# Optimization experiments

Hardware: AMD Instinct MI355X
Metric: run time of the kernel (lower is better)

Reference implementation:

```python
import jax, jax.numpy as jnp
import numpy as np

H = 8
D = 64
SCALER = 1.0 / np.sqrt(D).astype(np.float32)


def setup_inputs() -> dict:
    key = jax.random.key(0)
    k1, k2 = jax.random.split(key)
    B, N, C = 2, 256, 512
    x = jax.random.normal(k1, (B, N, C), dtype=jnp.float32)
    # Linear(C, 5C, bias=False): weight shape [5C, C], torch convention y = x @ W.T
    w = jax.random.normal(k2, (5 * C, C), dtype=jnp.float32) * 0.02
    return {"x": x, "w": w}


def reference(x, w):
    B, N, C = x.shape
    # projections: a, b, c, vj, vk each [B, H, N, D]
    wx = (x @ w.T).reshape(B, N, 5, H, D).transpose(2, 0, 3, 1, 4)
    a, b, c, vj, vk = wx[0], wx[1], wx[2], wx[3], wx[4]

    # three pairwise score matrices, each [B, H, N, N]
    X = jnp.einsum('bhjd,bhkd->bhjk', b, c) * SCALER
    Y = jnp.einsum('bhkd,bhid->bhki', c, a) * SCALER
    Z = jnp.einsum('bhid,bhjd->bhij', a, b) * SCALER

    # custom 3-way softmax stabilization: X uses global max over (j,k),
    # Y uses max over k (axis -2), Z uses max over j (axis -1)
    X = jnp.exp(X - jnp.max(X, axis=(-2, -1), keepdims=True))
    Y = jnp.exp(Y - jnp.max(Y, axis=-2, keepdims=True))
    Z = jnp.exp(Z - jnp.max(Z, axis=-1, keepdims=True))

    # Num_{bhid} = sum_{j,k} Z_ij * X_jk * vj_jd * Y_ki * vk_kd
    # (same math as the original 5D 'bhjkd'/'bhikd' chain, fused via einsum path)
    Num = jnp.einsum('bhij,bhjk,bhjd,bhki,bhkd->bhid', Z, X, vj, Y, vk)
    # Den_{bhi} = sum_{j,k} Z_ij * Y_ki * X_jk
    Den = jnp.einsum('bhij,bhki,bhjk->bhi', Z, Y, X) + 1e-9

    att = Num / Den[..., None]                     # [B, H, N, D]
    att = att.transpose(0, 2, 1, 3).reshape(B, N, C)
    return att
```

## Files before the change

kernel.cpp:

```cpp
#include <hip/hip_runtime.h>
#include <math.h>

#define Bn 2
#define Hn 8
#define Nn 256
#define Dn 64
#define BH 16
#define SCALER 0.125f

typedef _Float16 half8 __attribute__((ext_vector_type(8)));
typedef _Float16 half4 __attribute__((ext_vector_type(4)));
typedef float floatx4 __attribute__((ext_vector_type(4)));

__device__ __forceinline__ void split_f32(float v, _Float16& h, _Float16& l) {
    h = (_Float16)v;
    l = (_Float16)(v - (float)h);
}

__device__ __forceinline__ void split8(const float4& v0, const float4& v1,
                                       half8& h, half8& l) {
    const float vv[8] = {v0.x, v0.y, v0.z, v0.w, v1.x, v1.y, v1.z, v1.w};
    #pragma unroll
    for (int e = 0; e < 8; ++e) {
        _Float16 hh, ll;
        split_f32(vv[e], hh, ll);
        h[e] = hh; l[e] = ll;
    }
}

__device__ __forceinline__ void gload_lds16(const float* g, void* lds_base) {
    __builtin_amdgcn_global_load_lds(
        (const __attribute__((address_space(1))) unsigned int*)g,
        (__attribute__((address_space(3))) unsigned int*)lds_base, 16, 0, 0);
}

__global__ __launch_bounds__(256) void split2_kernel(
    const float* __restrict__ x, const float* __restrict__ w,
    _Float16* __restrict__ xh, _Float16* __restrict__ xl,
    _Float16* __restrict__ wh, _Float16* __restrict__ wl) {
    const int b = blockIdx.x;
    const float* src;
    _Float16 *hp, *lp;
    int idx;
    if (b < 256) {
        idx = (b * 256 + threadIdx.x) * 4;
        src = x; hp = xh; lp = xl;
    } else {
        idx = ((b - 256) * 256 + threadIdx.x) * 4;
        src = w; hp = wh; lp = wl;
    }
    const float4 v = *(const float4*)(src + idx);
    half4 hh, ll;
    _Float16 a2, b2;
    split_f32(v.x, a2, b2); hh[0] = a2; ll[0] = b2;
    split_f32(v.y, a2, b2); hh[1] = a2; ll[1] = b2;
    split_f32(v.z, a2, b2); hh[2] = a2; ll[2] = b2;
    split_f32(v.w, a2, b2); hh[3] = a2; ll[3] = b2;
    *(half4*)(hp + idx) = hh;
    *(half4*)(lp + idx) = ll;
}

__global__ __launch_bounds__(256) void proj_mfma(
    const _Float16* __restrict__ xh, const _Float16* __restrict__ xl,
    const _Float16* __restrict__ wh, const _Float16* __restrict__ wl,
    float* __restrict__ P32) {
    const int m0 = blockIdx.x * 64;
    const int r0 = blockIdx.y * 64;
    const int t = threadIdx.x;
    const int w = t >> 6, l = t & 63;
    const int lr = l & 15, kk8 = (l >> 4) * 8;

    floatx4 acc[4];
    #pragma unroll
    for (int ni = 0; ni < 4; ++ni) acc[ni] = (floatx4){0.f, 0.f, 0.f, 0.f};

    const int arow = m0 + w * 16 + lr;
    for (int kt = 0; kt < 16; ++kt) {
        const int k0 = kt * 32 + kk8;
        const half8 ah = *(const half8*)(xh + arow * 512 + k0);
        const half8 al = *(const half8*)(xl + arow * 512 + k0);
        half8 bhv[4], blv[4];
        #pragma unroll
        for (int ni = 0; ni < 4; ++ni) {
            const int wr = r0 + ni * 16 + lr;
            bhv[ni] = *(const half8*)(wh + wr * 512 + k0);
            blv[ni] = *(const half8*)(wl + wr * 512 + k0);
        }
        #pragma unroll
        for (int ni = 0; ni < 4; ++ni)
            acc[ni] = __builtin_amdgcn_mfma_f32_16x16x32_f16(ah, bhv[ni], acc[ni], 0, 0, 0);
        #pragma unroll
        for (int ni = 0; ni < 4; ++ni)
            acc[ni] = __builtin_amdgcn_mfma_f32_16x16x32_f16(ah, blv[ni], acc[ni], 0, 0, 0);
        #pragma unroll
        for (int ni = 0; ni < 4; ++ni)
            acc[ni] = __builtin_amdgcn_mfma_f32_16x16x32_f16(al, bhv[ni], acc[ni], 0, 0, 0);
    }
    const int rbase = (l >> 4) * 4;
    #pragma unroll
    for (int ni = 0; ni < 4; ++ni) {
        const int rcol = r0 + ni * 16 + lr;
        const int s = rcol >> 9, h = (rcol >> 6) & 7, d = rcol & 63;
        #pragma unroll
        for (int r = 0; r < 4; ++r) {
            const int m = m0 + w * 16 + rbase + r;
            const int b = m >> 8, n = m & 255;
            P32[(((s * 2 + b) * 8 + h) * 256 + n) * 64 + d] = acc[ni][r];
        }
    }
}

__global__ __launch_bounds__(256) void score_vkt(
    const float* __restrict__ P32,
    _Float16* __restrict__ Xsh, _Float16* __restrict__ Xsl,
    float* __restrict__ Yt, float* __restrict__ Z, float* __restrict__ vkT) {
    const int bh = blockIdx.x, mat = blockIdx.y;
    const int t = threadIdx.x;
    if (mat == 3) {
        const int idx0 = blockIdx.z * 2048 + t * 8;
        const int d = idx0 >> 8, k0 = idx0 & 255;
        const float* src = P32 + (4 * 16 + bh) * 16384;
        float4 o0, o1;
        o0.x = src[(k0 + 0) * 64 + d]; o0.y = src[(k0 + 1) * 64 + d];
        o0.z = src[(k0 + 2) * 64 + d]; o0.w = src[(k0 + 3) * 64 + d];
        o1.x = src[(k0 + 4) * 64 + d]; o1.y = src[(k0 + 5) * 64 + d];
        o1.z = src[(k0 + 6) * 64 + d]; o1.w = src[(k0 + 7) * 64 + d];
        *(float4*)(vkT + (bh * 64 + d) * 256 + k0) = o0;
        *(float4*)(vkT + (bh * 64 + d) * 256 + k0 + 4) = o1;
        return;
    }
    const int i0 = (blockIdx.z >> 2) * 128;
    const int j0 = (blockIdx.z & 3) * 64;
    const int w = t >> 6, l = t & 63;
    const int lr = l & 15, kk8 = (l >> 4) * 8;
    const float* A;
    const float* Bm;
    if (mat == 0)      { A = P32 + (1 * 16 + bh) * 16384; Bm = P32 + (2 * 16 + bh) * 16384; }
    else if (mat == 1) { A = P32 + (0 * 16 + bh) * 16384; Bm = P32 + (2 * 16 + bh) * 16384; }
    else               { A = P32 + (0 * 16 + bh) * 16384; Bm = P32 + (1 * 16 + bh) * 16384; }

    floatx4 acc[2][4];
    #pragma unroll
    for (int mi = 0; mi < 2; ++mi)
        #pragma unroll
        for (int ni = 0; ni < 4; ++ni) acc[mi][ni] = (floatx4){0.f, 0.f, 0.f, 0.f};

    for (int kt = 0; kt < 2; ++kt) {
        const int k0 = kt * 32 + kk8;
        half8 ah[2], al[2], bh8[4], bl8[4];
        #pragma unroll
        for (int mi = 0; mi < 2; ++mi) {
            const int row = i0 + w * 32 + mi * 16 + lr;
            const float4 v0 = *(const float4*)(A + row * 64 + k0);
            const float4 v1 = *(const float4*)(A + row * 64 + k0 + 4);
            split8(v0, v1, ah[mi], al[mi]);
        }
        #pragma unroll
        for (int ni = 0; ni < 4; ++ni) {
            const int row = j0 + ni * 16 + lr;
            const float4 v0 = *(const float4*)(Bm + row * 64 + k0);
            const float4 v1 = *(const float4*)(Bm + row * 64 + k0 + 4);
            split8(v0, v1, bh8[ni], bl8[ni]);
        }
        #pragma unroll
        for (int mi = 0; mi < 2; ++mi)
            #pragma unroll
            for (int ni = 0; ni < 4; ++ni)
                acc[mi][ni] = __builtin_amdgcn_mfma_f32_16x16x32_f16(ah[mi], bh8[ni], acc[mi][ni], 0, 0, 0);
        #pragma unroll
        for (int mi = 0; mi < 2; ++mi)
            #pragma unroll
            for (int ni = 0; ni < 4; ++ni)
                acc[mi][ni] = __builtin_amdgcn_mfma_f32_16x16x32_f16(ah[mi], bl8[ni], acc[mi][ni], 0, 0, 0);
        #pragma unroll
        for (int mi = 0; mi < 2; ++mi)
            #pragma unroll
            for (int ni = 0; ni < 4; ++ni)
                acc[mi][ni] = __builtin_amdgcn_mfma_f32_16x16x32_f16(al[mi], bh8[ni], acc[mi][ni], 0, 0, 0);
    }
    const int rbase = (l >> 4) * 4;
    #pragma unroll
    for (int mi = 0; mi < 2; ++mi)
        #pragma unroll
        for (int ni = 0; ni < 4; ++ni)
            #pragma unroll
            for (int r = 0; r < 4; ++r) {
                const int row = i0 + w * 32 + mi * 16 + rbase + r;
                const int col = j0 + ni * 16 + lr;
                const float e = expf(acc[mi][ni][r] * SCALER);
                if (mat == 0) {
                    const int idx = (bh * 256 + row) * 256 + col;
                    _Float16 hh, ll; split_f32(e, hh, ll);
                    Xsh[idx] = hh; Xsl[idx] = ll;
                } else if (mat == 1) {
                    Yt[bh * 65536 + row * 256 + col] = e;
                } else {
                    Z[bh * 65536 + row * 256 + col] = e;
                }
            }
}

__global__ __launch_bounds__(256) void den_mfma(
    const float* __restrict__ Yt, const _Float16* __restrict__ Xh,
    const _Float16* __restrict__ Xl, const float* __restrict__ Z,
    float* __restrict__ Den) {
    const int bh = blockIdx.x;
    const int ibase = blockIdx.y * 16;
    const int t = threadIdx.x;
    const int w = t >> 6, l = t & 63;
    const int lr = l & 15, ks = l >> 4, kk8 = ks * 8;
    const float* Ytp = Yt + bh * 65536;
    const _Float16* Xhp = Xh + bh * 65536;
    const _Float16* Xlp = Xl + bh * 65536;

    floatx4 acc[4];
    #pragma unroll
    for (int q = 0; q < 4; ++q) acc[q] = (floatx4){0.f, 0.f, 0.f, 0.f};

    for (int kt = 0; kt < 8; ++kt) {
        const int k0 = kt * 32 + kk8;
        half8 ah, al;
        {
            const float4 v0 = *(const float4*)(Ytp + (ibase + lr) * 256 + k0);
            const float4 v1 = *(const float4*)(Ytp + (ibase + lr) * 256 + k0 + 4);
            split8(v0, v1, ah, al);
        }
        half8 bh8[4], bl8[4];
        #pragma unroll
        for (int q = 0; q < 4; ++q) {
            const int jt = w * 4 + q;
            bh8[q] = *(const half8*)(Xhp + (jt * 16 + lr) * 256 + k0);
            bl8[q] = *(const half8*)(Xlp + (jt * 16 + lr) * 256 + k0);
        }
        #pragma unroll
        for (int q = 0; q < 4; ++q)
            acc[q] = __builtin_amdgcn_mfma_f32_16x16x32_f16(ah, bh8[q], acc[q], 0, 0, 0);
        #pragma unroll
        for (int q = 0; q < 4; ++q)
            acc[q] = __builtin_amdgcn_mfma_f32_16x16x32_f16(ah, bl8[q], acc[q], 0, 0, 0);
        #pragma unroll
        for (int q = 0; q < 4; ++q)
            acc[q] = __builtin_amdgcn_mfma_f32_16x16x32_f16(al, bh8[q], acc[q], 0, 0, 0);
    }
    __shared__ float redS[4][16];
    float dp[4] = {0.f, 0.f, 0.f, 0.f};
    const float* Zp = Z + (bh * 256 + ibase) * 256;
    #pragma unroll
    for (int q = 0; q < 4; ++q) {
        const int jt = w * 4 + q;
        #pragma unroll
        for (int r = 0; r < 4; ++r)
            dp[r] += acc[q][r] * Zp[(ks * 4 + r) * 256 + jt * 16 + lr];
    }
    #pragma unroll
    for (int r = 0; r < 4; ++r) {
        float s = dp[r];
        s += __shfl_xor(s, 1); s += __shfl_xor(s, 2);
        s += __shfl_xor(s, 4); s += __shfl_xor(s, 8);
        if (lr == 0) redS[w][ks * 4 + r] = s;
    }
    __syncthreads();
    if (t < 16)
        Den[bh * 256 + ibase + t] =
            redS[0][t] + redS[1][t] + redS[2][t] + redS[3][t] + 1e-9f;
}

__global__ __launch_bounds__(256, 2) void attn_mfma(
    const _Float16* __restrict__ Xh, const _Float16* __restrict__ Xl,
    const float* __restrict__ Yt, const float* __restrict__ Z,
    const float* __restrict__ vkT, const float* __restrict__ P32,
    const float* __restrict__ Den, float* __restrict__ out) {
    const int id = (blockIdx.x & 7) * 256 + (blockIdx.x >> 3);
    const int bh = id >> 7;
    const int i0 = (id & 127) * 2;
    const int t = threadIdx.x;
    const int w = t >> 6, l = t & 63;
    const int lr = l & 15, ks = l >> 4, kk8 = ks * 8;

    __shared__ float yiS[2][256], ziS[2][256];
    __shared__ float RAW[2][2048];
    __shared__ _Float16 BhS[2][2][2048], BlS[2][2][2048];
    float (*redN)[2][64] = reinterpret_cast<float (*)[2][64]>(&yiS[0][0]);

    yiS[0][t] = Yt[(bh * 256 + i0) * 256 + t];
    yiS[1][t] = Yt[(bh * 256 + i0 + 1) * 256 + t];
    ziS[0][t] = Z[(bh * 256 + i0) * 256 + t];
    ziS[1][t] = Z[(bh * 256 + i0 + 1) * 256 + t];

    const _Float16* Xhp = Xh + bh * 65536;
    const _Float16* Xlp = Xl + bh * 65536;
    const float* vkp = vkT + bh * 16384;
    const float* vj = P32 + (3 * 16 + bh) * 16384;

    floatx4 acc[4][8];
    #pragma unroll
    for (int mi = 0; mi < 4; ++mi)
        #pragma unroll
        for (int ct = 0; ct < 8; ++ct) acc[mi][ct] = (floatx4){0.f, 0.f, 0.f, 0.f};

    const int bi = t >> 7;
    const int bd = (t >> 1) & 63;
    const int hf = t & 1;
    const int bs2 = hf * 2;

    auto STAGE = [&](int kt) {
        const int k0 = (kt & 7) * 32;
        const int buf = kt & 1;
        #pragma unroll
        for (int q = 0; q < 2; ++q) {
            const int u = q * 256 + t;
            const int g = u >> 7, ubd = (u & 127) >> 1, uhf = u & 1;
            const float* gp = vkp + ubd * 256 + k0 + uhf * 16 + g * 4;
            void* lp = (char*)&RAW[buf][0] + q * 4096 + w * 1024;
            gload_lds16(gp, lp);
        }
    };
    auto BSTORE = [&](int kt) {
        const int buf = kt & 1;
        const float* yrow = &yiS[bi][(kt & 7) * 32 + bs2 * 8];
        float4 V[4];
        #pragma unroll
        for (int g = 0; g < 4; ++g)
            V[g] = *(float4*)&RAW[buf][g * 512 + bd * 8 + hf * 4];
        #pragma unroll
        for (int g = 0; g < 2; ++g) {
            const float4 y0 = *(const float4*)(yrow + g * 8);
            const float4 y1 = *(const float4*)(yrow + g * 8 + 4);
            const float4 v0 = V[g * 2], v1 = V[g * 2 + 1];
            const float pv[8] = {v0.x * y0.x, v0.y * y0.y, v0.z * y0.z, v0.w * y0.w,
                                 v1.x * y1.x, v1.y * y1.y, v1.z * y1.z, v1.w * y1.w};
            half8 hv, lv;
            #pragma unroll
            for (int e = 0; e < 8; ++e) {
                _Float16 hh, ll;
                split_f32(pv[e], hh, ll);
                hv[e] = hh; lv[e] = ll;
            }
            const int off = ((bd * 4 + bs2 + g) ^ ((bd >> 1) & 7)) * 8;
            *(half8*)&BhS[buf][bi][off] = hv;
            *(half8*)&BlS[buf][bi][off] = lv;
        }
    };
    auto LOADA = [&](half8* AH, half8* AL, int kt) {
        const int k0 = (kt & 7) * 32 + kk8;
        #pragma unroll
        for (int mi = 0; mi < 4; ++mi) {
            const int row = w * 64 + mi * 16 + lr;
            AH[mi] = *(const half8*)(Xhp + row * 256 + k0);
            AL[mi] = *(const half8*)(Xlp + row * 256 + k0);
        }
    };
    auto MFMA_STEP = [&](half8* AH, half8* AL, int buf) {
        __builtin_amdgcn_s_setprio(1);
        #pragma unroll
        for (int ct = 0; ct < 8; ++ct) {
            const int ii = ct >> 2;
            const int dd = (ct & 3) * 16 + lr;
            const int off = ((dd * 4 + ks) ^ ((dd >> 1) & 7)) * 8;
            const half8 bhf = *(const half8*)&BhS[buf][ii][off];
            const half8 blf = *(const half8*)&BlS[buf][ii][off];
            #pragma unroll
            for (int mi = 0; mi < 4; ++mi)
                acc[mi][ct] = __builtin_amdgcn_mfma_f32_16x16x32_f16(AH[mi], bhf, acc[mi][ct], 0, 0, 0);
            #pragma unroll
            for (int mi = 0; mi < 4; ++mi)
                acc[mi][ct] = __builtin_amdgcn_mfma_f32_16x16x32_f16(AH[mi], blf, acc[mi][ct], 0, 0, 0);
            #pragma unroll
            for (int mi = 0; mi < 4; ++mi)
                acc[mi][ct] = __builtin_amdgcn_mfma_f32_16x16x32_f16(AL[mi], bhf, acc[mi][ct], 0, 0, 0);
        }
        __builtin_amdgcn_s_setprio(0);
    };

    half8 A0h[4], A0l[4], A1h[4], A1l[4];

    STAGE(0);
    STAGE(1);
    LOADA(A0h, A0l, 0);
    asm volatile("s_waitcnt vmcnt(10)" ::: "memory");
    __builtin_amdgcn_sched_barrier(0);
    asm volatile("s_waitcnt lgkmcnt(0)" ::: "memory");
    __builtin_amdgcn_s_barrier();
    BSTORE(0);
    asm volatile("s_waitcnt lgkmcnt(0)" ::: "memory");
    __builtin_amdgcn_s_barrier();

    #pragma unroll 1
    for (int kq = 0; kq < 4; ++kq) {
        const int kt = kq * 2;
        STAGE(kt + 2);
        LOADA(A1h, A1l, kt + 1);
        MFMA_STEP(A0h, A0l, 0);
        asm volatile("s_waitcnt vmcnt(18)" ::: "memory");
        __builtin_amdgcn_sched_barrier(0);
        BSTORE(kt + 1);
        asm volatile("s_waitcnt lgkmcnt(0)" ::: "memory");
        __builtin_amdgcn_s_barrier();
        STAGE(kt + 3);
        LOADA(A0h, A0l, kt + 2);
        MFMA_STEP(A1h, A1l, 1);
        if (kq < 3) {
            asm volatile("s_waitcnt vmcnt(18)" ::: "memory");
            __builtin_amdgcn_sched_barrier(0);
            BSTORE(kt + 2);
            asm volatile("s_waitcnt lgkmcnt(0)" ::: "memory");
            __builtin_amdgcn_s_barrier();
        }
    }

    float z0[16], z1[16];
    #pragma unroll
    for (int mi = 0; mi < 4; ++mi)
        #pragma unroll
        for (int r = 0; r < 4; ++r) {
            const int j = w * 64 + mi * 16 + ks * 4 + r;
            z0[mi * 4 + r] = ziS[0][j];
            z1[mi * 4 + r] = ziS[1][j];
        }
    #pragma unroll
    for (int dt = 0; dt < 4; ++dt) {
        float n0 = 0.f, n1 = 0.f;
        #pragma unroll
        for (int mi = 0; mi < 4; ++mi)
            #pragma unroll
            for (int r = 0; r < 4; ++r) {
                const int j = w * 64 + mi * 16 + ks * 4 + r;
                const float v = vj[j * 64 + dt * 16 + lr];
                n0 += acc[mi][dt][r] * z0[mi * 4 + r] * v;
                n1 += acc[mi][dt + 4][r] * z1[mi * 4 + r] * v;
            }
        n0 += __shfl_xor(n0, 16); n0 += __shfl_xor(n0, 32);
        n1 += __shfl_xor(n1, 16); n1 += __shfl_xor(n1, 32);
        if (l < 16) {
            redN[w][0][dt * 16 + l] = n0;
            redN[w][1][dt * 16 + l] = n1;
        }
    }
    __syncthreads();
    if (t < 128) {
        const int ih = t >> 6, d = t & 63;
        const float num = redN[0][ih][d] + redN[1][ih][d] +
                          redN[2][ih][d] + redN[3][ih][d];
        const int i = i0 + ih;
        const float den = Den[bh * 256 + i];
        out[((bh >> 3) * 256 + i) * 512 + (bh & 7) * 64 + d] = num / den;
    }
}

extern "C" void kernel_launch(void* const* d_in, const int* in_sizes, int n_in,
                              void* d_out, int out_size, void* d_ws, size_t ws_size,
                              hipStream_t stream) {
    const float* x = (const float*)d_in[0];
    const float* w = (const float*)d_in[1];
    float* out = (float*)d_out;

    float* ws = (float*)d_ws;
    float* P32 = ws;
    float* U = ws + 1310720;
    _Float16* xh = (_Float16*)U;
    _Float16* xl = xh + 262144;
    _Float16* wh = xl + 262144;
    _Float16* wl = wh + 1310720;
    _Float16* Xsh = (_Float16*)U;
    _Float16* Xsl = Xsh + 1048576;
    float* Yt = U + 1048576;
    float* Z = Yt + 1048576;
    float* vkT = Z + 1048576;
    float* Den = vkT + 262144;

    split2_kernel<<<1536, 256, 0, stream>>>(x, w, xh, xl, wh, wl);
    proj_mfma<<<dim3(8, 40), 256, 0, stream>>>(xh, xl, wh, wl, P32);
    score_vkt<<<dim3(16, 4, 8), 256, 0, stream>>>(P32, Xsh, Xsl, Yt, Z, vkT);
    den_mfma<<<dim3(16, 16), 256, 0, stream>>>(Yt, Xsh, Xsl, Z, Den);
    attn_mfma<<<2048, 256, 0, stream>>>(Xsh, Xsl, Yt, Z, vkT, P32, Den, out);
}
```

Baseline: 180.1 us.

## Split attn_mfma output head dimension across two blocks to raise occupancy

Each attn_mfma block now computes only half of the D=64 output columns (32), so the grid doubles to 4096 blocks. Per-block accumulators, the shared B tiles and the vk staging shrink by half, and launch bounds rise to 3 waves per SIMD to improve latency hiding. The cost is that the X (A operand) tile loads, the Z/Y row loads and the high/low split are now repeated by twice as many blocks, which doubles A-side traffic relative to MFMA work.

```diff
diff --git a/kernel.cpp b/kernel.cpp
--- a/kernel.cpp
+++ b/kernel.cpp
@@ -265,22 +265,24 @@
             redS[0][t] + redS[1][t] + redS[2][t] + redS[3][t] + 1e-9f;
 }
 
-__global__ __launch_bounds__(256, 2) void attn_mfma(
+__global__ __launch_bounds__(256, 3) void attn_mfma(
     const _Float16* __restrict__ Xh, const _Float16* __restrict__ Xl,
     const float* __restrict__ Yt, const float* __restrict__ Z,
     const float* __restrict__ vkT, const float* __restrict__ P32,
     const float* __restrict__ Den, float* __restrict__ out) {
-    const int id = (blockIdx.x & 7) * 256 + (blockIdx.x >> 3);
-    const int bh = id >> 7;
-    const int i0 = (id & 127) * 2;
+    const int id = (blockIdx.x & 7) * 512 + (blockIdx.x >> 3);
+    const int bh = id >> 8;
+    const int rest = id & 255;
+    const int dh = rest >> 7;
+    const int i0 = (rest & 127) * 2;
     const int t = threadIdx.x;
     const int w = t >> 6, l = t & 63;
     const int lr = l & 15, ks = l >> 4, kk8 = ks * 8;
 
     __shared__ float yiS[2][256], ziS[2][256];
-    __shared__ float RAW[2][2048];
-    __shared__ _Float16 BhS[2][2][2048], BlS[2][2][2048];
-    float (*redN)[2][64] = reinterpret_cast<float (*)[2][64]>(&yiS[0][0]);
+    __shared__ float RAW[2][1024];
+    __shared__ _Float16 BhS[2][2][1024], BlS[2][2][1024];
+    __shared__ float redN[4][2][32];
 
     yiS[0][t] = Yt[(bh * 256 + i0) * 256 + t];
     yiS[1][t] = Yt[(bh * 256 + i0 + 1) * 256 + t];
@@ -289,57 +291,46 @@
 
     const _Float16* Xhp = Xh + bh * 65536;
     const _Float16* Xlp = Xl + bh * 65536;
-    const float* vkp = vkT + bh * 16384;
+    const float* vkp = vkT + (bh * 64 + dh * 32) * 256;
     const float* vj = P32 + (3 * 16 + bh) * 16384;
 
-    floatx4 acc[4][8];
+    floatx4 acc[4][4];
     #pragma unroll
     for (int mi = 0; mi < 4; ++mi)
         #pragma unroll
-        for (int ct = 0; ct < 8; ++ct) acc[mi][ct] = (floatx4){0.f, 0.f, 0.f, 0.f};
+        for (int ct = 0; ct < 4; ++ct) acc[mi][ct] = (floatx4){0.f, 0.f, 0.f, 0.f};
 
     const int bi = t >> 7;
-    const int bd = (t >> 1) & 63;
-    const int hf = t & 1;
-    const int bs2 = hf * 2;
+    const int bd = (t >> 2) & 31;
+    const int sl = t & 3;
+    const int uhf = sl >> 1, gb = (sl & 1) * 2;
 
     auto STAGE = [&](int kt) {
         const int k0 = (kt & 7) * 32;
         const int buf = kt & 1;
-        #pragma unroll
-        for (int q = 0; q < 2; ++q) {
-            const int u = q * 256 + t;
-            const int g = u >> 7, ubd = (u & 127) >> 1, uhf = u & 1;
-            const float* gp = vkp + ubd * 256 + k0 + uhf * 16 + g * 4;
-            void* lp = (char*)&RAW[buf][0] + q * 4096 + w * 1024;
-            gload_lds16(gp, lp);
-        }
+        const float* gp = vkp + (l >> 1) * 256 + k0 + (l & 1) * 16 + w * 4;
+        void* lp = (char*)&RAW[buf][0] + w * 1024;
+        gload_lds16(gp, lp);
     };
     auto BSTORE = [&](int kt) {
         const int buf = kt & 1;
-        const float* yrow = &yiS[bi][(kt & 7) * 32 + bs2 * 8];
-        float4 V[4];
-        #pragma unroll
-        for (int g = 0; g < 4; ++g)
-            V[g] = *(float4*)&RAW[buf][g * 512 + bd * 8 + hf * 4];
-        #pragma unroll
-        for (int g = 0; g < 2; ++g) {
-            const float4 y0 = *(const float4*)(yrow + g * 8);
-            const float4 y1 = *(const float4*)(yrow + g * 8 + 4);
-            const float4 v0 = V[g * 2], v1 = V[g * 2 + 1];
-            const float pv[8] = {v0.x * y0.x, v0.y * y0.y, v0.z * y0.z, v0.w * y0.w,
-                                 v1.x * y1.x, v1.y * y1.y, v1.z * y1.z, v1.w * y1.w};
-            half8 hv, lv;
-            #pragma unroll
-            for (int e = 0; e < 8; ++e) {
-                _Float16 hh, ll;
-                split_f32(pv[e], hh, ll);
-                hv[e] = hh; lv[e] = ll;
-            }
-            const int off = ((bd * 4 + bs2 + g) ^ ((bd >> 1) & 7)) * 8;
-            *(half8*)&BhS[buf][bi][off] = hv;
-            *(half8*)&BlS[buf][bi][off] = lv;
-        }
+        const float* yrow = &yiS[bi][(kt & 7) * 32 + sl * 8];
+        const float4 v0 = *(float4*)&RAW[buf][(gb * 64 + bd * 2 + uhf) * 4];
+        const float4 v1 = *(float4*)&RAW[buf][((gb + 1) * 64 + bd * 2 + uhf) * 4];
+        const float4 y0 = *(const float4*)(yrow);
+        const float4 y1 = *(const float4*)(yrow + 4);
+        const float pv[8] = {v0.x * y0.x, v0.y * y0.y, v0.z * y0.z, v0.w * y0.w,
+                             v1.x * y1.x, v1.y * y1.y, v1.z * y1.z, v1.w * y1.w};
+        half8 hv, lv;
+        #pragma unroll
+        for (int e = 0; e < 8; ++e) {
+            _Float16 hh, ll;
+            split_f32(pv[e], hh, ll);
+            hv[e] = hh; lv[e] = ll;
+        }
+        const int off = ((bd * 4 + sl) ^ ((bd >> 1) & 7)) * 8;
+        *(half8*)&BhS[buf][bi][off] = hv;
+        *(half8*)&BlS[buf][bi][off] = lv;
     };
     auto LOADA = [&](half8* AH, half8* AL, int kt) {
         const int k0 = (kt & 7) * 32 + kk8;
@@ -353,9 +344,9 @@
     auto MFMA_STEP = [&](half8* AH, half8* AL, int buf) {
         __builtin_amdgcn_s_setprio(1);
         #pragma unroll
-        for (int ct = 0; ct < 8; ++ct) {
-            const int ii = ct >> 2;
-            const int dd = (ct & 3) * 16 + lr;
+        for (int ct = 0; ct < 4; ++ct) {
+            const int ii = ct >> 1;
+            const int dd = (ct & 1) * 16 + lr;
             const int off = ((dd * 4 + ks) ^ ((dd >> 1) & 7)) * 8;
             const half8 bhf = *(const half8*)&BhS[buf][ii][off];
             const half8 blf = *(const half8*)&BlS[buf][ii][off];
@@ -377,7 +368,7 @@
     STAGE(0);
     STAGE(1);
     LOADA(A0h, A0l, 0);
-    asm volatile("s_waitcnt vmcnt(10)" ::: "memory");
+    asm volatile("s_waitcnt vmcnt(9)" ::: "memory");
     __builtin_amdgcn_sched_barrier(0);
     asm volatile("s_waitcnt lgkmcnt(0)" ::: "memory");
     __builtin_amdgcn_s_barrier();
@@ -391,7 +382,7 @@
         STAGE(kt + 2);
         LOADA(A1h, A1l, kt + 1);
         MFMA_STEP(A0h, A0l, 0);
-        asm volatile("s_waitcnt vmcnt(18)" ::: "memory");
+        asm volatile("s_waitcnt vmcnt(17)" ::: "memory");
         __builtin_amdgcn_sched_barrier(0);
         BSTORE(kt + 1);
         asm volatile("s_waitcnt lgkmcnt(0)" ::: "memory");
@@ -400,7 +391,7 @@
         LOADA(A0h, A0l, kt + 2);
         MFMA_STEP(A1h, A1l, 1);
         if (kq < 3) {
-            asm volatile("s_waitcnt vmcnt(18)" ::: "memory");
+            asm volatile("s_waitcnt vmcnt(17)" ::: "memory");
             __builtin_amdgcn_sched_barrier(0);
             BSTORE(kt + 2);
             asm volatile("s_waitcnt lgkmcnt(0)" ::: "memory");
@@ -418,16 +409,16 @@
             z1[mi * 4 + r] = ziS[1][j];
         }
     #pragma unroll
-    for (int dt = 0; dt < 4; ++dt) {
+    for (int dt = 0; dt < 2; ++dt) {
         float n0 = 0.f, n1 = 0.f;
         #pragma unroll
         for (int mi = 0; mi < 4; ++mi)
             #pragma unroll
             for (int r = 0; r < 4; ++r) {
                 const int j = w * 64 + mi * 16 + ks * 4 + r;
-                const float v = vj[j * 64 + dt * 16 + lr];
+                const float v = vj[j * 64 + dh * 32 + dt * 16 + lr];
                 n0 += acc[mi][dt][r] * z0[mi * 4 + r] * v;
-                n1 += acc[mi][dt + 4][r] * z1[mi * 4 + r] * v;
+                n1 += acc[mi][2 + dt][r] * z1[mi * 4 + r] * v;
             }
         n0 += __shfl_xor(n0, 16); n0 += __shfl_xor(n0, 32);
         n1 += __shfl_xor(n1, 16); n1 += __shfl_xor(n1, 32);
@@ -437,13 +428,13 @@
         }
     }
     __syncthreads();
-    if (t < 128) {
-        const int ih = t >> 6, d = t & 63;
-        const float num = redN[0][ih][d] + redN[1][ih][d] +
-                          redN[2][ih][d] + redN[3][ih][d];
+    if (t < 64) {
+        const int ih = t >> 5, dloc = t & 31;
+        const float num = redN[0][ih][dloc] + redN[1][ih][dloc] +
+                          redN[2][ih][dloc] + redN[3][ih][dloc];
         const int i = i0 + ih;
         const float den = Den[bh * 256 + i];
-        out[((bh >> 3) * 256 + i) * 512 + (bh & 7) * 64 + d] = num / den;
+        out[((bh >> 3) * 256 + i) * 512 + (bh & 7) * 64 + dh * 32 + dloc] = num / den;
     }
 }
 
@@ -472,5 +463,5 @@
     proj_mfma<<<dim3(8, 40), 256, 0, stream>>>(xh, xl, wh, wl, P32);
     score_vkt<<<dim3(16, 4, 8), 256, 0, stream>>>(P32, Xsh, Xsl, Yt, Z, vkT);
     den_mfma<<<dim3(16, 16), 256, 0, stream>>>(Yt, Xsh, Xsl, Z, Den);
-    attn_mfma<<<2048, 256, 0, stream>>>(Xsh, Xsl, Yt, Z, vkT, P32, Den, out);
-}
+    attn_mfma<<<4096, 256, 0, stream>>>(Xsh, Xsl, Yt, Z, vkT, P32, Den, out);
+}
```

Measured after the change: 262.8 us. 45.9% more time.
